# Performance work log

Hardware: AMD Instinct MI355X
Metric: run time of the kernel (lower is better)

Reference implementation:

```python
import jax, jax.numpy as jnp
import numpy as np

# Module config (matches init_kwargs)
N, D1, D2, BW, K = 8, 1024, 1024, 4, 4
D = D1 * D2
B = 4096
TEMPERATURE = 1.0


def setup_inputs() -> dict:
    key = jax.random.key(0)
    ks = jax.random.split(key, 6)
    x = jax.random.normal(ks[0], (B, N, D1), dtype=jnp.float32)
    # learned parameters (kaiming-ish normal init; exact init does not matter for correctness baseline)
    U = jax.random.normal(ks[1], (N, D, K), dtype=jnp.float32)
    V = jax.random.normal(ks[2], (BW, D, K), dtype=jnp.float32)
    scale = jax.random.normal(ks[3], (N, 1), dtype=jnp.float32)
    biasq = jax.random.normal(ks[4], (N, 1), dtype=jnp.float32)
    bias = jax.random.normal(ks[5], (N, D2), dtype=jnp.float32)
    return {"x": x, "U": U, "V": V, "scale": scale, "biasq": biasq, "bias": bias}


def reference(x, U, V, scale, biasq, bias):
    # twopow = [2^0, ..., 2^{bw-1}] (non-learned buffer)
    twopow = 2.0 ** jnp.arange(BW, dtype=jnp.float32)
    # CP contraction: Theta[n, b, d] = sum_k U[n,d,k] * V[b,d,k]
    Theta = jnp.einsum('ndk,bdk->nbd', U, V)  # (N, BW, D)
    # sigmoid with temperature T, input clamped to [-10, 10]
    soft_binary = jax.nn.sigmoid(jnp.clip(TEMPERATURE * Theta, -10.0, 10.0))
    # bit-weighted sum -> soft integer per weight element
    integer = jnp.einsum('nbd,b->nd', soft_binary, twopow)  # (N, D)
    # dequantize: scale * (integer - biasq - 2^bw)
    w = scale * (integer - biasq - 2.0 ** BW)  # (N, D)
    w = w.reshape(N, D1, D2)
    # batched per-ensemble-member GEMM: act[b,n,l] = sum_d x[b,n,d] * w[n,d,l]
    act = jnp.einsum('bnd,ndl->bnl', x, w) + bias  # bias broadcasts (N, D2)
    return act
```

## Files before the change

kernel.cpp:

```cpp
#include <hip/hip_runtime.h>


typedef __attribute__((ext_vector_type(8))) short short8;
typedef __attribute__((ext_vector_type(4))) float f32x4;
typedef __attribute__((ext_vector_type(4))) unsigned short ushort4v;

__device__ __forceinline__ unsigned short f2bf(float f) {
  union { float f; unsigned u; } a; a.f = f;
  unsigned u = a.u;
  u += 0x7fffu + ((u >> 16) & 1u);
  return (unsigned short)(u >> 16);
}

__global__ __launch_bounds__(256) void xcast_kernel(
    const float4* __restrict__ X4, ushort4v* __restrict__ Xb4) {
  const size_t idx = (size_t)blockIdx.x * 256 + threadIdx.x;
  const float4 v = X4[idx];
  const size_t flat = idx << 2;
  const int d1 = (int)(flat & 1023);
  const size_t nb = flat >> 10;
  const int nn = (int)(nb & 7);
  const size_t b = nb >> 3;
  ushort4v o;
  o.x = f2bf(v.x); o.y = f2bf(v.y); o.z = f2bf(v.z); o.w = f2bf(v.w);
  Xb4[(((size_t)nn << 22) + (b << 10) + (size_t)d1) >> 2] = o;
}

__global__ __launch_bounds__(256) void wgen_kernel(
    const float4* __restrict__ U4, const float4* __restrict__ V4,
    const float* __restrict__ scale, const float* __restrict__ biasq,
    unsigned short* __restrict__ Wt) {
  __shared__ float tiles[8][32][33];
  const int t = threadIdx.x;
  const int d1_0 = blockIdx.x * 32;
  const int d2_0 = blockIdx.y * 32;
#pragma unroll
  for (int i = 0; i < 4; i++) {
    const int e = t + 256 * i;
    const int r = e >> 5, c = e & 31;
    const size_t d = (size_t)(d1_0 + r) * 1024 + (size_t)(d2_0 + c);
    float4 u[8];
#pragma unroll
    for (int nn = 0; nn < 8; nn++) u[nn] = U4[((size_t)nn << 20) + d];
    float integ[8];
#pragma unroll
    for (int nn = 0; nn < 8; nn++) integ[nn] = 0.f;
#pragma unroll
    for (int b = 0; b < 4; b++) {
      const float4 v = V4[((size_t)b << 20) + d];
      const float pw = (float)(1 << b);
#pragma unroll
      for (int nn = 0; nn < 8; nn++) {
        float th = u[nn].x * v.x + u[nn].y * v.y + u[nn].z * v.z + u[nn].w * v.w;
        th = fminf(10.f, fmaxf(-10.f, th));
        integ[nn] += pw / (1.f + __expf(-th));
      }
    }
#pragma unroll
    for (int nn = 0; nn < 8; nn++) tiles[nn][r][c] = integ[nn];
  }
  __syncthreads();
#pragma unroll
  for (int i = 0; i < 4; i++) {
    const int e = t + 256 * i;
    const int orow = e >> 5, oc = e & 31;
#pragma unroll
    for (int nn = 0; nn < 8; nn++) {
      const float wval = scale[nn] * (tiles[nn][oc][orow] - biasq[nn] - 16.f);
      Wt[((size_t)nn << 20) + (size_t)(d2_0 + orow) * 1024 + (size_t)(d1_0 + oc)] =
          f2bf(wval);
    }
  }
}

#define AS1(p) ((const __attribute__((address_space(1))) void*)(p))
#define AS3(p) ((__attribute__((address_space(3))) void*)(p))

__global__ __launch_bounds__(256) void gemm_kernel(
    const unsigned short* __restrict__ Xb,
    const unsigned short* __restrict__ Wt,
    const float* __restrict__ bias,
    float* __restrict__ out) {
  __shared__ unsigned short As[128 * 64];
  __shared__ unsigned short Bs[128 * 64];
  const int t = threadIdx.x;
  const int wv = t >> 6;
  const int ln = t & 63;
  const int n = blockIdx.z;
  const int bm0 = blockIdx.x * 128;
  const int bn0 = blockIdx.y * 128;

  const unsigned short* Ag = Xb + ((size_t)n << 22);
  const unsigned short* Bg = Wt + ((size_t)n << 20);

  const int sr = wv * 8 + (ln >> 3);
  const int sk = (((ln & 7) ^ (sr & 7)) * 8);
  const unsigned short* ag = Ag + (size_t)(bm0 + sr) * 1024 + sk;
  const unsigned short* bg = Bg + (size_t)(bn0 + sr) * 1024 + sk;
  unsigned short* lA = As + wv * 512;
  unsigned short* lB = Bs + wv * 512;

  const int wm = wv >> 1, wn = wv & 1;
  const int lm = ln & 15;
  const int cq = ln >> 4;
  const int sw = lm & 7;
  const unsigned short* a_rd = As + (wm * 64 + lm) * 64;
  const unsigned short* b_rd = Bs + (wn * 64 + lm) * 64;

  f32x4 acc[4][4];
#pragma unroll
  for (int i = 0; i < 4; i++)
#pragma unroll
    for (int j = 0; j < 4; j++) acc[i][j] = (f32x4){0.f, 0.f, 0.f, 0.f};

  for (int k0 = 0; k0 < 1024; k0 += 64) {
#pragma unroll
    for (int r = 0; r < 4; r++) {
      __builtin_amdgcn_global_load_lds(AS1(ag + (size_t)(32 * r) * 1024 + k0),
                                       AS3(lA + r * 2048), 16, 0, 0);
      __builtin_amdgcn_global_load_lds(AS1(bg + (size_t)(32 * r) * 1024 + k0),
                                       AS3(lB + r * 2048), 16, 0, 0);
    }
    __syncthreads();
#pragma unroll
    for (int half = 0; half < 2; half++) {
      const int off = ((half * 4 + cq) ^ sw) * 8;
      short8 af[4], bfr[4];
#pragma unroll
      for (int i = 0; i < 4; i++) af[i] = *(const short8*)(a_rd + i * 1024 + off);
#pragma unroll
      for (int j = 0; j < 4; j++) bfr[j] = *(const short8*)(b_rd + j * 1024 + off);
#pragma unroll
      for (int i = 0; i < 4; i++)
#pragma unroll
        for (int j = 0; j < 4; j++)
          acc[i][j] = __builtin_amdgcn_mfma_f32_16x16x32_bf16(af[i], bfr[j],
                                                              acc[i][j], 0, 0, 0);
    }
    __syncthreads();
  }

  const int q = ln >> 4;
  const int row0 = bm0 + wm * 64 + q * 4;
  const int col0 = bn0 + wn * 64 + lm;
  float bv[4];
#pragma unroll
  for (int j = 0; j < 4; j++) bv[j] = bias[n * 1024 + col0 + j * 16];
#pragma unroll
  for (int i = 0; i < 4; i++) {
#pragma unroll
    for (int r = 0; r < 4; r++) {
      const int row = row0 + i * 16 + r;
      float* op = out + ((size_t)row * 8 + (size_t)n) * 1024;
#pragma unroll
      for (int j = 0; j < 4; j++) op[col0 + j * 16] = acc[i][j][r] + bv[j];
    }
  }
}

extern "C" void kernel_launch(void* const* d_in, const int* in_sizes, int n_in,
                              void* d_out, int out_size, void* d_ws, size_t ws_size,
                              hipStream_t stream) {
  const float* x     = (const float*)d_in[0];
  const float* U     = (const float*)d_in[1];
  const float* V     = (const float*)d_in[2];
  const float* scale = (const float*)d_in[3];
  const float* biasq = (const float*)d_in[4];
  const float* bias  = (const float*)d_in[5];
  float* out = (float*)d_out;

  unsigned short* Xb = (unsigned short*)d_ws;
  unsigned short* Wt = (unsigned short*)((char*)d_ws + (size_t)67108864);

  xcast_kernel<<<32768, 256, 0, stream>>>((const float4*)x, (ushort4v*)Xb);
  wgen_kernel<<<dim3(32, 32), 256, 0, stream>>>((const float4*)U, (const float4*)V,
                                                scale, biasq, Wt);
  gemm_kernel<<<dim3(32, 8, 8), 256, 0, stream>>>(Xb, Wt, bias, out);
}
```

Measured before the change: 469.1 us.

## Load GEMM fragments directly from global memory with register double-buffering

The LDS staging path (global_load_lds plus block-wide barriers) is replaced by per-wave loads of MFMA fragments straight from global memory into registers, with the next K-slice prefetched while the current one is multiplied. The goal is to remove the LDS round-trips and __syncthreads stalls. In exchange, operands are no longer shared within the block, so each wave pulls its own A/B rows from global memory and L2, and each lane's 16-byte loads are strided across rows, so coalescing gets worse.

Result: slower. 614.1 us (+30.9%).

```diff
diff --git a/kernel.cpp b/kernel.cpp
--- a/kernel.cpp
+++ b/kernel.cpp
@@ -73,39 +73,25 @@
   }
 }
 
-#define AS1(p) ((const __attribute__((address_space(1))) void*)(p))
-#define AS3(p) ((__attribute__((address_space(3))) void*)(p))
-
 __global__ __launch_bounds__(256) void gemm_kernel(
     const unsigned short* __restrict__ Xb,
     const unsigned short* __restrict__ Wt,
     const float* __restrict__ bias,
     float* __restrict__ out) {
-  __shared__ unsigned short As[128 * 64];
-  __shared__ unsigned short Bs[128 * 64];
   const int t = threadIdx.x;
   const int wv = t >> 6;
   const int ln = t & 63;
+  const int wm = wv >> 1, wn = wv & 1;
+  const int lm = ln & 15;
+  const int cq = ln >> 4;
   const int n = blockIdx.z;
   const int bm0 = blockIdx.x * 128;
   const int bn0 = blockIdx.y * 128;
 
-  const unsigned short* Ag = Xb + ((size_t)n << 22);
-  const unsigned short* Bg = Wt + ((size_t)n << 20);
-
-  const int sr = wv * 8 + (ln >> 3);
-  const int sk = (((ln & 7) ^ (sr & 7)) * 8);
-  const unsigned short* ag = Ag + (size_t)(bm0 + sr) * 1024 + sk;
-  const unsigned short* bg = Bg + (size_t)(bn0 + sr) * 1024 + sk;
-  unsigned short* lA = As + wv * 512;
-  unsigned short* lB = Bs + wv * 512;
-
-  const int wm = wv >> 1, wn = wv & 1;
-  const int lm = ln & 15;
-  const int cq = ln >> 4;
-  const int sw = lm & 7;
-  const unsigned short* a_rd = As + (wm * 64 + lm) * 64;
-  const unsigned short* b_rd = Bs + (wn * 64 + lm) * 64;
+  const unsigned short* A0 =
+      Xb + ((size_t)n << 22) + (size_t)(bm0 + wm * 64 + lm) * 1024 + cq * 8;
+  const unsigned short* B0 =
+      Wt + ((size_t)n << 20) + (size_t)(bn0 + wn * 64 + lm) * 1024 + cq * 8;
 
   f32x4 acc[4][4];
 #pragma unroll
@@ -113,34 +99,38 @@
 #pragma unroll
     for (int j = 0; j < 4; j++) acc[i][j] = (f32x4){0.f, 0.f, 0.f, 0.f};
 
-  for (int k0 = 0; k0 < 1024; k0 += 64) {
+  short8 a[4], b[4], an[4], bn2[4];
 #pragma unroll
-    for (int r = 0; r < 4; r++) {
-      __builtin_amdgcn_global_load_lds(AS1(ag + (size_t)(32 * r) * 1024 + k0),
-                                       AS3(lA + r * 2048), 16, 0, 0);
-      __builtin_amdgcn_global_load_lds(AS1(bg + (size_t)(32 * r) * 1024 + k0),
-                                       AS3(lB + r * 2048), 16, 0, 0);
-    }
-    __syncthreads();
+  for (int i = 0; i < 4; i++) a[i] = *(const short8*)(A0 + (size_t)i * 16384);
 #pragma unroll
-    for (int half = 0; half < 2; half++) {
-      const int off = ((half * 4 + cq) ^ sw) * 8;
-      short8 af[4], bfr[4];
+  for (int j = 0; j < 4; j++) b[j] = *(const short8*)(B0 + (size_t)j * 16384);
+
 #pragma unroll
-      for (int i = 0; i < 4; i++) af[i] = *(const short8*)(a_rd + i * 1024 + off);
+  for (int kk = 0; kk < 31; kk++) {
+    const int ko = (kk + 1) * 32;
 #pragma unroll
-      for (int j = 0; j < 4; j++) bfr[j] = *(const short8*)(b_rd + j * 1024 + off);
+    for (int i = 0; i < 4; i++)
+      an[i] = *(const short8*)(A0 + (size_t)i * 16384 + ko);
 #pragma unroll
-      for (int i = 0; i < 4; i++)
+    for (int j = 0; j < 4; j++)
+      bn2[j] = *(const short8*)(B0 + (size_t)j * 16384 + ko);
 #pragma unroll
-        for (int j = 0; j < 4; j++)
-          acc[i][j] = __builtin_amdgcn_mfma_f32_16x16x32_bf16(af[i], bfr[j],
-                                                              acc[i][j], 0, 0, 0);
-    }
-    __syncthreads();
+    for (int i = 0; i < 4; i++)
+#pragma unroll
+      for (int j = 0; j < 4; j++)
+        acc[i][j] =
+            __builtin_amdgcn_mfma_f32_16x16x32_bf16(a[i], b[j], acc[i][j], 0, 0, 0);
+#pragma unroll
+    for (int i = 0; i < 4; i++) { a[i] = an[i]; b[i] = bn2[i]; }
   }
+#pragma unroll
+  for (int i = 0; i < 4; i++)
+#pragma unroll
+    for (int j = 0; j < 4; j++)
+      acc[i][j] =
+          __builtin_amdgcn_mfma_f32_16x16x32_bf16(a[i], b[j], acc[i][j], 0, 0, 0);
 
-  const int q = ln >> 4;
+  const int q = cq;
   const int row0 = bm0 + wm * 64 + q * 4;
   const int col0 = bn0 + wn * 64 + lm;
   float bv[4];
```

## Fuse fp32-to-bf16 cast of x into GEMM A-tile load; vectorize W stores

Applied to the files above, without the earlier changes.

Drops the separate xcast kernel. The GEMM now reads fp32 x directly through registers, converts it to bf16 and writes the swizzled A tile into LDS. This removes a full write and re-read of a 64MB bf16 intermediate and one kernel launch. In exchange, the A path becomes synchronous register loads instead of async global_load_lds, and each x element is read 8 times as fp32 (once per N-tile block), which doubles A-side traffic per reread. The wgen transpose store is also widened to 4-element vector writes.

After: 453.4 us. 1.03x faster.

```diff
diff --git a/kernel.cpp b/kernel.cpp
--- a/kernel.cpp
+++ b/kernel.cpp
@@ -1,9 +1,11 @@
 #include <hip/hip_runtime.h>
+#include <hip/hip_bf16.h>
 
 
 typedef __attribute__((ext_vector_type(8))) short short8;
 typedef __attribute__((ext_vector_type(4))) float f32x4;
 typedef __attribute__((ext_vector_type(4))) unsigned short ushort4v;
+typedef __attribute__((ext_vector_type(2))) unsigned int uint2v;
 
 __device__ __forceinline__ unsigned short f2bf(float f) {
   union { float f; unsigned u; } a; a.f = f;
@@ -12,18 +14,10 @@
   return (unsigned short)(u >> 16);
 }
 
-__global__ __launch_bounds__(256) void xcast_kernel(
-    const float4* __restrict__ X4, ushort4v* __restrict__ Xb4) {
-  const size_t idx = (size_t)blockIdx.x * 256 + threadIdx.x;
-  const float4 v = X4[idx];
-  const size_t flat = idx << 2;
-  const int d1 = (int)(flat & 1023);
-  const size_t nb = flat >> 10;
-  const int nn = (int)(nb & 7);
-  const size_t b = nb >> 3;
-  ushort4v o;
-  o.x = f2bf(v.x); o.y = f2bf(v.y); o.z = f2bf(v.z); o.w = f2bf(v.w);
-  Xb4[(((size_t)nn << 22) + (b << 10) + (size_t)d1) >> 2] = o;
+__device__ __forceinline__ unsigned pk2(float a, float b) {
+  __hip_bfloat162 h = __float22bfloat162_rn(make_float2(a, b));
+  union { __hip_bfloat162 h; unsigned u; } c; c.h = h;
+  return c.u;
 }
 
 __global__ __launch_bounds__(256) void wgen_kernel(
@@ -60,16 +54,18 @@
     for (int nn = 0; nn < 8; nn++) tiles[nn][r][c] = integ[nn];
   }
   __syncthreads();
+  const int orow = t >> 3;
+  const int oc0 = (t & 7) * 4;
 #pragma unroll
-  for (int i = 0; i < 4; i++) {
-    const int e = t + 256 * i;
-    const int orow = e >> 5, oc = e & 31;
-#pragma unroll
-    for (int nn = 0; nn < 8; nn++) {
-      const float wval = scale[nn] * (tiles[nn][oc][orow] - biasq[nn] - 16.f);
-      Wt[((size_t)nn << 20) + (size_t)(d2_0 + orow) * 1024 + (size_t)(d1_0 + oc)] =
-          f2bf(wval);
-    }
+  for (int nn = 0; nn < 8; nn++) {
+    const float sc = scale[nn], bq = biasq[nn];
+    ushort4v o;
+    o.x = f2bf(sc * (tiles[nn][oc0 + 0][orow] - bq - 16.f));
+    o.y = f2bf(sc * (tiles[nn][oc0 + 1][orow] - bq - 16.f));
+    o.z = f2bf(sc * (tiles[nn][oc0 + 2][orow] - bq - 16.f));
+    o.w = f2bf(sc * (tiles[nn][oc0 + 3][orow] - bq - 16.f));
+    *(ushort4v*)(Wt + ((size_t)nn << 20) + (size_t)(d2_0 + orow) * 1024 +
+                 (size_t)(d1_0 + oc0)) = o;
   }
 }
 
@@ -77,7 +73,7 @@
 #define AS3(p) ((__attribute__((address_space(3))) void*)(p))
 
 __global__ __launch_bounds__(256) void gemm_kernel(
-    const unsigned short* __restrict__ Xb,
+    const float* __restrict__ X,
     const unsigned short* __restrict__ Wt,
     const float* __restrict__ bias,
     float* __restrict__ out) {
@@ -90,14 +86,17 @@
   const int bm0 = blockIdx.x * 128;
   const int bn0 = blockIdx.y * 128;
 
-  const unsigned short* Ag = Xb + ((size_t)n << 22);
-  const unsigned short* Bg = Wt + ((size_t)n << 20);
+  const int ar = t >> 4;
+  const int f = t & 15;
+  const int a_cg = f >> 1;
+  const int a_half = f & 1;
+  const float* Ax = X + ((size_t)(bm0 + ar) * 8 + (size_t)n) * 1024 + f * 4;
+  unsigned short* wA = As + ar * 64 + ((a_cg ^ (ar & 7)) * 8) + a_half * 4;
 
   const int sr = wv * 8 + (ln >> 3);
   const int sk = (((ln & 7) ^ (sr & 7)) * 8);
-  const unsigned short* ag = Ag + (size_t)(bm0 + sr) * 1024 + sk;
-  const unsigned short* bg = Bg + (size_t)(bn0 + sr) * 1024 + sk;
-  unsigned short* lA = As + wv * 512;
+  const unsigned short* bg =
+      Wt + ((size_t)n << 20) + (size_t)(bn0 + sr) * 1024 + sk;
   unsigned short* lB = Bs + wv * 512;
 
   const int wm = wv >> 1, wn = wv & 1;
@@ -115,11 +114,22 @@
 
   for (int k0 = 0; k0 < 1024; k0 += 64) {
 #pragma unroll
-    for (int r = 0; r < 4; r++) {
-      __builtin_amdgcn_global_load_lds(AS1(ag + (size_t)(32 * r) * 1024 + k0),
-                                       AS3(lA + r * 2048), 16, 0, 0);
+    for (int r = 0; r < 4; r++)
       __builtin_amdgcn_global_load_lds(AS1(bg + (size_t)(32 * r) * 1024 + k0),
                                        AS3(lB + r * 2048), 16, 0, 0);
+#pragma unroll
+    for (int h2 = 0; h2 < 2; h2++) {
+      float4 av[4];
+#pragma unroll
+      for (int i = 0; i < 4; i++)
+        av[i] = *(const float4*)(Ax + k0 + (size_t)(h2 * 4 + i) * 131072);
+#pragma unroll
+      for (int i = 0; i < 4; i++) {
+        uint2v p;
+        p.x = pk2(av[i].x, av[i].y);
+        p.y = pk2(av[i].z, av[i].w);
+        *(uint2v*)(wA + (h2 * 4 + i) * 1024) = p;
+      }
     }
     __syncthreads();
 #pragma unroll
@@ -169,11 +179,9 @@
   const float* bias  = (const float*)d_in[5];
   float* out = (float*)d_out;
 
-  unsigned short* Xb = (unsigned short*)d_ws;
-  unsigned short* Wt = (unsigned short*)((char*)d_ws + (size_t)67108864);
+  unsigned short* Wt = (unsigned short*)d_ws;
 
-  xcast_kernel<<<32768, 256, 0, stream>>>((const float4*)x, (ushort4v*)Xb);
   wgen_kernel<<<dim3(32, 32), 256, 0, stream>>>((const float4*)U, (const float4*)V,
                                                 scale, biasq, Wt);
-  gemm_kernel<<<dim3(32, 8, 8), 256, 0, stream>>>(Xb, Wt, bias, out);
+  gemm_kernel<<<dim3(32, 8, 8), 256, 0, stream>>>(x, Wt, bias, out);
 }
```
